# Performance work log

Hardware: AMD Instinct MI355X
Metric: run time of the kernel (lower is better)

## Reference

```python
import jax, jax.numpy as jnp
import numpy as np


def setup_inputs() -> dict:
    key = jax.random.key(0)
    ks = jax.random.split(key, 8)
    B, N, H = 8, 64, 256
    nE, E = 256, 64
    HID, OUT = 512, 1
    s1 = 1.0 / np.sqrt(H + E)
    s2 = 1.0 / np.sqrt(HID)
    return {
        "h_all": jax.random.normal(ks[0], (B, N, H), dtype=jnp.float32),
        "e_feat": jax.random.normal(ks[1], (nE, E), dtype=jnp.float32),
        "W1": jax.random.normal(ks[2], (H + E, HID), dtype=jnp.float32) * s1,
        "b1": jnp.zeros((HID,), dtype=jnp.float32),
        "W2": jax.random.normal(ks[3], (HID, HID), dtype=jnp.float32) * s2,
        "b2": jnp.zeros((HID,), dtype=jnp.float32),
        "W3": jax.random.normal(ks[4], (HID, OUT), dtype=jnp.float32) * s2,
        "b3": jnp.zeros((OUT,), dtype=jnp.float32),
    }


def reference(h_all, e_feat, W1, b1, W2, b2, W3, b3):
    # Math == MLP(cat([expand(h), expand(e)], -1)) but computed via split
    # weights: cat([h,e]) @ W1 == h @ W1[:H] + e @ W1[H:], avoiding the
    # materialized [B,N,nE,H+E] concat tensor.
    H = h_all.shape[-1]
    Wh, We = W1[:H], W1[H:]
    h_part = jnp.einsum("bnh,hk->bnk", h_all, Wh)        # [B,N,HID]
    e_part = jnp.einsum("ed,dk->ek", e_feat, We)          # [nE,HID]
    x = h_part[:, :, None, :] + e_part[None, None, :, :] + b1  # [B,N,nE,HID]
    x = jax.nn.relu(x)
    x = jax.nn.relu(jnp.einsum("bnek,kj->bnej", x, W2) + b2)
    return jnp.einsum("bnek,ko->bneo", x, W3) + b3        # [B,N,nE,OUT]
```

## Files before the change

kernel.cpp:

```cpp
#include <hip/hip_runtime.h>
#include <hip/hip_bf16.h>


typedef __attribute__((ext_vector_type(8))) short bf16x8;
typedef __attribute__((ext_vector_type(16))) float f32x16;

static __device__ __forceinline__ ushort2 pk_bf16(float a, float b) {
  union { __hip_bfloat162 h; ushort2 u; } c;
  c.h = __float22bfloat162_rn(make_float2(a, b));
  return c.u;
}
static __device__ __forceinline__ float bf2f(unsigned short u) {
  union { unsigned int i; float f; } c;
  c.i = ((unsigned int)u) << 16;
  return c.f;
}

__global__ __launch_bounds__(256) void k_prep(
    const float* __restrict__ h_all, const float* __restrict__ e_feat,
    const float* __restrict__ W1, const float* __restrict__ b1,
    const float* __restrict__ W2,
    unsigned short* __restrict__ hpb, unsigned short* __restrict__ epb,
    unsigned short* __restrict__ w2f) {
  __shared__ float sm[64 * 68];
  const int t = threadIdx.x;
  const int b = blockIdx.x;

  if (b < 256) {
    const int r0 = b * 2;
    float (*hs)[256] = (float(*)[256])sm;
    hs[0][t] = h_all[(size_t)r0 * 256 + t];
    hs[1][t] = h_all[(size_t)(r0 + 1) * 256 + t];
    __syncthreads();
    float2 a0 = make_float2(0.f, 0.f), a1 = make_float2(0.f, 0.f);
    #pragma unroll 2
    for (int k = 0; k < 256; k += 4) {
      float2 w0 = *(const float2*)(W1 + (size_t)k * 512 + 2 * t);
      float2 w1 = *(const float2*)(W1 + (size_t)(k + 1) * 512 + 2 * t);
      float2 w2v = *(const float2*)(W1 + (size_t)(k + 2) * 512 + 2 * t);
      float2 w3v = *(const float2*)(W1 + (size_t)(k + 3) * 512 + 2 * t);
      float h00 = hs[0][k], h01 = hs[0][k + 1], h02 = hs[0][k + 2], h03 = hs[0][k + 3];
      float h10 = hs[1][k], h11 = hs[1][k + 1], h12 = hs[1][k + 2], h13 = hs[1][k + 3];
      a0.x = fmaf(h00, w0.x, a0.x); a0.y = fmaf(h00, w0.y, a0.y);
      a1.x = fmaf(h10, w0.x, a1.x); a1.y = fmaf(h10, w0.y, a1.y);
      a0.x = fmaf(h01, w1.x, a0.x); a0.y = fmaf(h01, w1.y, a0.y);
      a1.x = fmaf(h11, w1.x, a1.x); a1.y = fmaf(h11, w1.y, a1.y);
      a0.x = fmaf(h02, w2v.x, a0.x); a0.y = fmaf(h02, w2v.y, a0.y);
      a1.x = fmaf(h12, w2v.x, a1.x); a1.y = fmaf(h12, w2v.y, a1.y);
      a0.x = fmaf(h03, w3v.x, a0.x); a0.y = fmaf(h03, w3v.y, a0.y);
      a1.x = fmaf(h13, w3v.x, a1.x); a1.y = fmaf(h13, w3v.y, a1.y);
    }
    float2 bv = *(const float2*)(b1 + 2 * t);
    *(ushort2*)(hpb + (size_t)r0 * 512 + 2 * t) = pk_bf16(a0.x + bv.x, a0.y + bv.y);
    *(ushort2*)(hpb + (size_t)(r0 + 1) * 512 + 2 * t) = pk_bf16(a1.x + bv.x, a1.y + bv.y);
  } else if (b < 288) {
    const int r0 = (b - 256) * 8;
    sm[t] = e_feat[(size_t)r0 * 64 + t];
    sm[256 + t] = e_feat[(size_t)r0 * 64 + 256 + t];
    __syncthreads();
    float2 acc[8];
    #pragma unroll
    for (int i = 0; i < 8; ++i) acc[i] = make_float2(0.f, 0.f);
    for (int k = 0; k < 64; ++k) {
      float2 wv = *(const float2*)(W1 + (size_t)(256 + k) * 512 + 2 * t);
      #pragma unroll
      for (int i = 0; i < 8; ++i) {
        acc[i].x = fmaf(sm[i * 64 + k], wv.x, acc[i].x);
        acc[i].y = fmaf(sm[i * 64 + k], wv.y, acc[i].y);
      }
    }
    #pragma unroll
    for (int i = 0; i < 8; ++i)
      *(ushort2*)(epb + (size_t)(r0 + i) * 512 + 2 * t) = pk_bf16(acc[i].x, acc[i].y);
  } else {
    const int bbk = b - 288;
    const int k0 = (bbk >> 3) * 64;
    const int c0 = (bbk & 7) * 64;
    #pragma unroll
    for (int rr = 0; rr < 4; ++rr) {
      const int row = rr * 16 + (t >> 4);
      float4 v = *(const float4*)(W2 + (size_t)(k0 + row) * 512 + c0 + (t & 15) * 4);
      *(float4*)(&sm[row * 68 + (t & 15) * 4]) = v;
    }
    __syncthreads();
    #pragma unroll
    for (int s2 = 0; s2 < 2; ++s2) {
      const int s = t * 2 + s2;
      const int rec = s >> 6, l = s & 63;
      const int jg = (c0 >> 5) + (rec & 1);
      const int ks = (k0 >> 4) + (rec >> 1);
      const int cl = (rec & 1) * 32 + (l & 31);
      const int kl = (rec >> 1) * 16 + (l >> 5) * 8;
      union { ushort2 o[4]; uint4 v; } u;
      #pragma unroll
      for (int uu = 0; uu < 4; ++uu)
        u.o[uu] = pk_bf16(sm[(kl + 2 * uu) * 68 + cl], sm[(kl + 2 * uu + 1) * 68 + cl]);
      *(uint4*)(w2f + ((size_t)(jg * 32 + ks) * 64 + l) * 8) = u.v;
    }
  }
}

__global__ __launch_bounds__(512, 4) void k_main(
    const unsigned short* __restrict__ hpb, const unsigned short* __restrict__ epb,
    const unsigned short* __restrict__ w2f, const float* __restrict__ b2,
    const float* __restrict__ W3, const float* __restrict__ b3,
    float* __restrict__ out) {
  __shared__ unsigned short x1s[64 * 512];

  const int t = threadIdx.x;
  const int lane = t & 63;
  const int w = t >> 6;
  const int l31 = lane & 31, l5 = lane >> 5;
  const int bn = blockIdx.x >> 2;
  const int e0 = (blockIdx.x & 3) << 6;
  const int off = (blockIdx.x * 7) & 31;
  const unsigned short* hprow = hpb + (size_t)bn * 512;

  const unsigned short* wrec0 = w2f + (size_t)(w * 2) * 16384 + (size_t)lane * 8;
  const unsigned short* wrec1 = wrec0 + 16384;
  bf16x8 bb[2][2];
  bb[0][0] = *(const bf16x8*)(wrec0 + (size_t)off * 512);
  bb[0][1] = *(const bf16x8*)(wrec1 + (size_t)off * 512);
  bb[1][0] = *(const bf16x8*)(wrec0 + (size_t)((off + 1) & 31) * 512);
  bb[1][1] = *(const bf16x8*)(wrec1 + (size_t)((off + 1) & 31) * 512);

  {
    const int kk = t & 63;
    const int rbase = t >> 6;
    union { uint4 v; unsigned short s[8]; } hv, ev, ov;
    hv.v = *(const uint4*)(hprow + kk * 8);
    float hf[8];
    #pragma unroll
    for (int u = 0; u < 8; ++u) hf[u] = bf2f(hv.s[u]);
    #pragma unroll 4
    for (int rr = 0; rr < 8; ++rr) {
      const int r = rr * 8 + rbase;
      ev.v = *(const uint4*)(epb + (size_t)(e0 + r) * 512 + kk * 8);
      #pragma unroll
      for (int u = 0; u < 4; ++u) {
        ushort2 p = pk_bf16(fmaxf(bf2f(ev.s[2 * u]) + hf[2 * u], 0.f),
                            fmaxf(bf2f(ev.s[2 * u + 1]) + hf[2 * u + 1], 0.f));
        ov.s[2 * u] = p.x;
        ov.s[2 * u + 1] = p.y;
      }
      *(uint4*)(&x1s[r * 512 + (kk ^ (r & 7)) * 8]) = ov.v;
    }
  }
  __syncthreads();

  const int xr = l31 & 7;
  f32x16 acc[2][2] = {};
  #pragma unroll 4
  for (int ks = 0; ks < 32; ++ks) {
    const int cur = ks & 1;
    const int kr = (ks + off) & 31;
    const int kr2 = (ks + 2 + off) & 31;
    const int c0 = ((kr * 2 + l5) ^ xr) * 8;
    bf16x8 a0 = *(const bf16x8*)(&x1s[l31 * 512 + c0]);
    bf16x8 a1 = *(const bf16x8*)(&x1s[(l31 + 32) * 512 + c0]);
    acc[0][0] = __builtin_amdgcn_mfma_f32_32x32x16_bf16(a0, bb[cur][0], acc[0][0], 0, 0, 0);
    acc[1][0] = __builtin_amdgcn_mfma_f32_32x32x16_bf16(a1, bb[cur][0], acc[1][0], 0, 0, 0);
    acc[0][1] = __builtin_amdgcn_mfma_f32_32x32x16_bf16(a0, bb[cur][1], acc[0][1], 0, 0, 0);
    acc[1][1] = __builtin_amdgcn_mfma_f32_32x32x16_bf16(a1, bb[cur][1], acc[1][1], 0, 0, 0);
    bb[cur][0] = *(const bf16x8*)(wrec0 + (size_t)kr2 * 512);
    bb[cur][1] = *(const bf16x8*)(wrec1 + (size_t)kr2 * 512);
  }

  float part[2][16];
  #pragma unroll
  for (int rt = 0; rt < 2; ++rt)
    #pragma unroll
    for (int r = 0; r < 16; ++r) part[rt][r] = 0.f;
  #pragma unroll
  for (int ct = 0; ct < 2; ++ct) {
    const int n = w * 64 + ct * 32 + l31;
    const float b2v = b2[n], w3v = W3[n];
    #pragma unroll
    for (int rt = 0; rt < 2; ++rt)
      #pragma unroll
      for (int r = 0; r < 16; ++r)
        part[rt][r] = fmaf(fmaxf(acc[rt][ct][r] + b2v, 0.f), w3v, part[rt][r]);
  }
  #pragma unroll
  for (int rt = 0; rt < 2; ++rt)
    #pragma unroll
    for (int r = 0; r < 16; ++r) {
      float v = part[rt][r];
      v += __shfl_xor(v, 1);
      v += __shfl_xor(v, 2);
      v += __shfl_xor(v, 4);
      v += __shfl_xor(v, 8);
      v += __shfl_xor(v, 16);
      part[rt][r] = v;
    }
  __syncthreads();
  float* osum = (float*)x1s;
  if (l31 == 0) {
    #pragma unroll
    for (int rt = 0; rt < 2; ++rt)
      #pragma unroll
      for (int r = 0; r < 16; ++r)
        osum[w * 64 + rt * 32 + (r & 3) + 8 * (r >> 2) + 4 * l5] = part[rt][r];
  }
  __syncthreads();
  if (t < 64) {
    float s = b3[0];
    #pragma unroll
    for (int g = 0; g < 8; ++g) s += osum[g * 64 + t];
    out[(size_t)bn * 256 + e0 + t] = s;
  }
}

extern "C" void kernel_launch(void* const* d_in, const int* in_sizes, int n_in,
                              void* d_out, int out_size, void* d_ws, size_t ws_size,
                              hipStream_t stream) {
  const float* h_all  = (const float*)d_in[0];
  const float* e_feat = (const float*)d_in[1];
  const float* W1     = (const float*)d_in[2];
  const float* b1     = (const float*)d_in[3];
  const float* W2     = (const float*)d_in[4];
  const float* b2     = (const float*)d_in[5];
  const float* W3     = (const float*)d_in[6];
  const float* b3     = (const float*)d_in[7];
  float* out = (float*)d_out;

  unsigned short* hpb = (unsigned short*)d_ws;
  unsigned short* epb = hpb + 512 * 512;
  unsigned short* w2f = epb + 256 * 512;

  hipLaunchKernelGGL(k_prep, dim3(352), dim3(256), 0, stream,
                     h_all, e_feat, W1, b1, W2, hpb, epb, w2f);
  hipLaunchKernelGGL(k_main, dim3(2048), dim3(512), 0, stream,
                     hpb, epb, w2f, b2, W3, b3, out);
}
```

Before: 164.4 us.

## Double block tile to 128 edge rows with 16 waves and fragment-ordered LDS

Each block now handles 128 edge rows with 1024 threads (16 waves), split into two row groups sharing the same W2 column slices. The first-layer activations are written to LDS already in MFMA fragment order, so A loads become contiguous per-lane reads with no XOR swizzle. The aim is to halve the block count and per-block setup while reusing W2 register fragments across more rows. In exchange LDS per block doubles to 128 KB, which limits residency, and the 1024-thread launch bound adds register pressure.

```diff
diff --git a/kernel.cpp b/kernel.cpp
--- a/kernel.cpp
+++ b/kernel.cpp
@@ -100,23 +100,25 @@
   }
 }
 
-__global__ __launch_bounds__(512, 4) void k_main(
+__global__ __launch_bounds__(1024, 4) void k_main(
     const unsigned short* __restrict__ hpb, const unsigned short* __restrict__ epb,
     const unsigned short* __restrict__ w2f, const float* __restrict__ b2,
     const float* __restrict__ W3, const float* __restrict__ b3,
     float* __restrict__ out) {
-  __shared__ unsigned short x1s[64 * 512];
+  __shared__ unsigned short x1s[128 * 512];
 
   const int t = threadIdx.x;
   const int lane = t & 63;
   const int w = t >> 6;
   const int l31 = lane & 31, l5 = lane >> 5;
-  const int bn = blockIdx.x >> 2;
-  const int e0 = (blockIdx.x & 3) << 6;
+  const int cg = w & 7;
+  const int rt2 = w >> 3;
+  const int bn = blockIdx.x >> 1;
+  const int e0 = (blockIdx.x & 1) << 7;
   const int off = (blockIdx.x * 7) & 31;
   const unsigned short* hprow = hpb + (size_t)bn * 512;
 
-  const unsigned short* wrec0 = w2f + (size_t)(w * 2) * 16384 + (size_t)lane * 8;
+  const unsigned short* wrec0 = w2f + (size_t)(cg * 2) * 16384 + (size_t)lane * 8;
   const unsigned short* wrec1 = wrec0 + 16384;
   bf16x8 bb[2][2];
   bb[0][0] = *(const bf16x8*)(wrec0 + (size_t)off * 512);
@@ -125,39 +127,37 @@
   bb[1][1] = *(const bf16x8*)(wrec1 + (size_t)((off + 1) & 31) * 512);
 
   {
-    const int kk = t & 63;
-    const int rbase = t >> 6;
-    union { uint4 v; unsigned short s[8]; } hv, ev, ov;
-    hv.v = *(const uint4*)(hprow + kk * 8);
-    float hf[8];
-    #pragma unroll
-    for (int u = 0; u < 8; ++u) hf[u] = bf2f(hv.s[u]);
-    #pragma unroll 4
-    for (int rr = 0; rr < 8; ++rr) {
-      const int r = rr * 8 + rbase;
-      ev.v = *(const uint4*)(epb + (size_t)(e0 + r) * 512 + kk * 8);
+    #pragma unroll
+    for (int i = 0; i < 8; ++i) {
+      const int rec = w * 8 + i;
+      const int rt = rec >> 5;
+      const int ks = rec & 31;
+      const int k0 = ks * 16 + l5 * 8;
+      const int er = e0 + rt * 32 + l31;
+      union { uint4 v; unsigned short s[8]; } hv, ev, ov;
+      hv.v = *(const uint4*)(hprow + k0);
+      ev.v = *(const uint4*)(epb + (size_t)er * 512 + k0);
       #pragma unroll
       for (int u = 0; u < 4; ++u) {
-        ushort2 p = pk_bf16(fmaxf(bf2f(ev.s[2 * u]) + hf[2 * u], 0.f),
-                            fmaxf(bf2f(ev.s[2 * u + 1]) + hf[2 * u + 1], 0.f));
+        ushort2 p = pk_bf16(fmaxf(bf2f(hv.s[2 * u]) + bf2f(ev.s[2 * u]), 0.f),
+                            fmaxf(bf2f(hv.s[2 * u + 1]) + bf2f(ev.s[2 * u + 1]), 0.f));
         ov.s[2 * u] = p.x;
         ov.s[2 * u + 1] = p.y;
       }
-      *(uint4*)(&x1s[r * 512 + (kk ^ (r & 7)) * 8]) = ov.v;
+      *(uint4*)(&x1s[(size_t)rec * 512 + lane * 8]) = ov.v;
     }
   }
   __syncthreads();
 
-  const int xr = l31 & 7;
+  const int arec0 = (rt2 * 2) * 32;
   f32x16 acc[2][2] = {};
   #pragma unroll 4
   for (int ks = 0; ks < 32; ++ks) {
     const int cur = ks & 1;
     const int kr = (ks + off) & 31;
     const int kr2 = (ks + 2 + off) & 31;
-    const int c0 = ((kr * 2 + l5) ^ xr) * 8;
-    bf16x8 a0 = *(const bf16x8*)(&x1s[l31 * 512 + c0]);
-    bf16x8 a1 = *(const bf16x8*)(&x1s[(l31 + 32) * 512 + c0]);
+    bf16x8 a0 = *(const bf16x8*)(&x1s[(size_t)(arec0 + kr) * 512 + lane * 8]);
+    bf16x8 a1 = *(const bf16x8*)(&x1s[(size_t)(arec0 + 32 + kr) * 512 + lane * 8]);
     acc[0][0] = __builtin_amdgcn_mfma_f32_32x32x16_bf16(a0, bb[cur][0], acc[0][0], 0, 0, 0);
     acc[1][0] = __builtin_amdgcn_mfma_f32_32x32x16_bf16(a1, bb[cur][0], acc[1][0], 0, 0, 0);
     acc[0][1] = __builtin_amdgcn_mfma_f32_32x32x16_bf16(a0, bb[cur][1], acc[0][1], 0, 0, 0);
@@ -173,7 +173,7 @@
     for (int r = 0; r < 16; ++r) part[rt][r] = 0.f;
   #pragma unroll
   for (int ct = 0; ct < 2; ++ct) {
-    const int n = w * 64 + ct * 32 + l31;
+    const int n = cg * 64 + ct * 32 + l31;
     const float b2v = b2[n], w3v = W3[n];
     #pragma unroll
     for (int rt = 0; rt < 2; ++rt)
@@ -203,10 +203,12 @@
         osum[w * 64 + rt * 32 + (r & 3) + 8 * (r >> 2) + 4 * l5] = part[rt][r];
   }
   __syncthreads();
-  if (t < 64) {
+  if (t < 128) {
+    const int rh = t >> 6;
+    const int rl = t & 63;
     float s = b3[0];
     #pragma unroll
-    for (int g = 0; g < 8; ++g) s += osum[g * 64 + t];
+    for (int g = 0; g < 8; ++g) s += osum[(rh * 8 + g) * 64 + rl];
     out[(size_t)bn * 256 + e0 + t] = s;
   }
 }
@@ -230,6 +232,6 @@
 
   hipLaunchKernelGGL(k_prep, dim3(352), dim3(256), 0, stream,
                      h_all, e_feat, W1, b1, W2, hpb, epb, w2f);
-  hipLaunchKernelGGL(k_main, dim3(2048), dim3(512), 0, stream,
+  hipLaunchKernelGGL(k_main, dim3(1024), dim3(1024), 0, stream,
                      hpb, epb, w2f, b2, W3, b3, out);
 }
```

New measurement: 183.8 us. +11.8%, slower.
